# Performance work log

Measured on AMD Instinct MI355X. Metric: run time of the kernel, lower is better.

Reference implementation:

```python
import jax, jax.numpy as jnp
import numpy as np

USER_VOCAB = 1_000_000
MOVIE_VOCAB = 100_000
EMB_DIM = 64
BATCH = 65536
H1, H2 = 256, 128  # over_arch_layer_sizes


def setup_inputs() -> dict:
    key = jax.random.key(0)
    ks = jax.random.split(key, 10)
    inv = 1.0 / np.sqrt(EMB_DIM)
    return {
        "user_ids": jax.random.randint(ks[0], (BATCH,), 0, USER_VOCAB),
        "movie_ids": jax.random.randint(ks[1], (BATCH,), 0, MOVIE_VOCAB),
        "emb_user": jax.random.normal(ks[2], (USER_VOCAB, EMB_DIM), jnp.float32) * inv,
        "emb_movie": jax.random.normal(ks[3], (MOVIE_VOCAB, EMB_DIM), jnp.float32) * inv,
        "W1": jax.random.normal(ks[4], (EMB_DIM, H1), jnp.float32) * (1.0 / np.sqrt(EMB_DIM)),
        "b1": jnp.zeros((H1,), jnp.float32),
        "W2": jax.random.normal(ks[5], (H1, H2), jnp.float32) * (1.0 / np.sqrt(H1)),
        "b2": jnp.zeros((H2,), jnp.float32),
        "W3": jax.random.normal(ks[6], (H2, 1), jnp.float32) * (1.0 / np.sqrt(H2)),
        "b3": jnp.zeros((1,), jnp.float32),
    }


def reference(user_ids, movie_ids, emb_user, emb_movie, W1, b1, W2, b2, W3, b3):
    B = user_ids.shape[0]
    # sparse gather per feature (hotness = 1)
    eu = emb_user[user_ids]    # [B, D]
    em = emb_movie[movie_ids]  # [B, D]
    # concat jagged outputs along rows, matching torch.cat(..., dim=0)
    x = jnp.concatenate([eu, em], axis=0)  # [2B, D]
    h = jax.nn.relu(x @ W1 + b1)
    h = jax.nn.relu(h @ W2 + b2)
    p = h @ W3 + b3                        # [2B, 1]
    # view(num_features, batch).t().sum(-1) -> sum over features per sample
    return p.reshape(2, B).sum(axis=0)     # [B]
```

## Files before the change

kernel.cpp:

```cpp
#include <hip/hip_runtime.h>


typedef __attribute__((ext_vector_type(8))) short bf16x8;
typedef __attribute__((ext_vector_type(4))) float f32x4;

__device__ __forceinline__ unsigned int cvt_pk(float lo, float hi) {
  unsigned int r;
  asm("v_cvt_pk_bf16_f32 %0, %1, %2" : "=v"(r) : "v"(lo), "v"(hi));
  return r;
}

__global__ __launch_bounds__(512, 2) void movielens_mlp(
    const int* __restrict__ uids, const int* __restrict__ mids,
    const float* __restrict__ EU, const float* __restrict__ EM,
    const float* __restrict__ W1, const float* __restrict__ B1,
    const float* __restrict__ W2, const float* __restrict__ B2,
    const float* __restrict__ W3, const float* __restrict__ B3,
    float* __restrict__ out) {
  __shared__ __align__(16) unsigned short w1f[16 * 2 * 512];
  __shared__ __align__(16) unsigned short w2f[8 * 8 * 512];

  const int tid = threadIdx.x;
  const int lane = tid & 63, wv = tid >> 6;
  const int m = lane & 15, g = lane >> 4;

  const int sbase = blockIdx.x * 256 + wv * 32;
  const int su = sbase + m, sv = su + 16;

  const float* rp[4];
  rp[0] = EU + (size_t)uids[su] * 64;
  rp[1] = EU + (size_t)uids[sv] * 64;
  rp[2] = EM + (size_t)mids[su] * 64;
  rp[3] = EM + (size_t)mids[sv] * 64;
  float4 xr[4][2][2];
#pragma unroll
  for (int mt = 0; mt < 4; ++mt)
#pragma unroll
    for (int kt = 0; kt < 2; ++kt) {
      xr[mt][kt][0] = *(const float4*)(rp[mt] + kt * 32 + 8 * g);
      xr[mt][kt][1] = *(const float4*)(rp[mt] + kt * 32 + 8 * g + 4);
    }

  {
    const int u = tid & 63;
#pragma unroll
    for (int pass = 0; pass < 2; ++pass) {
      const int qd = (tid >> 6) + 8 * pass;
      const float* src = W1 + (qd * 4) * 256 + 4 * u;
      const float4 r0 = *(const float4*)(src);
      const float4 r1 = *(const float4*)(src + 256);
      const float4 r2 = *(const float4*)(src + 512);
      const float4 r3 = *(const float4*)(src + 768);
      const float c0[4] = {r0.x, r0.y, r0.z, r0.w};
      const float c1[4] = {r1.x, r1.y, r1.z, r1.w};
      const float c2[4] = {r2.x, r2.y, r2.z, r2.w};
      const float c3[4] = {r3.x, r3.y, r3.z, r3.w};
      const int kt = qd >> 3, gg = (qd >> 1) & 3, bo = (qd & 1) * 4;
#pragma unroll
      for (int p = 0; p < 4; ++p) {
        const int n = 4 * u + p;
        const int hq = n >> 5, cl = n & 31;
        const int nt = (cl >> 2) & 1, mm = 4 * (cl >> 3) + (cl & 3);
        const int fi = hq * 4 + nt * 2 + kt;
        uint2 pk;
        pk.x = cvt_pk(c0[p], c1[p]);
        pk.y = cvt_pk(c2[p], c3[p]);
        *(uint2*)&w1f[fi * 512 + (gg * 16 + mm) * 8 + bo] = pk;
      }
    }
    const int u2 = tid & 31;
#pragma unroll
    for (int pass = 0; pass < 4; ++pass) {
      const int qd = (tid >> 5) + 16 * pass;
      const float* src = W2 + (qd * 4) * 128 + 4 * u2;
      const float4 r0 = *(const float4*)(src);
      const float4 r1 = *(const float4*)(src + 128);
      const float4 r2 = *(const float4*)(src + 256);
      const float4 r3 = *(const float4*)(src + 384);
      const float c0[4] = {r0.x, r0.y, r0.z, r0.w};
      const float c1[4] = {r1.x, r1.y, r1.z, r1.w};
      const float c2[4] = {r2.x, r2.y, r2.z, r2.w};
      const float c3[4] = {r3.x, r3.y, r3.z, r3.w};
      const int hq2 = qd >> 3, gg = (qd >> 1) & 3, bo = (qd & 1) * 4;
#pragma unroll
      for (int p = 0; p < 4; ++p) {
        const int n = 4 * u2 + p, nt2 = n >> 4, mm = n & 15;
        uint2 pk;
        pk.x = cvt_pk(c0[p], c1[p]);
        pk.y = cvt_pk(c2[p], c3[p]);
        *(uint2*)&w2f[(nt2 * 8 + hq2) * 512 + (gg * 16 + mm) * 8 + bo] = pk;
      }
    }
  }

  bf16x8 xf[4][2];
#pragma unroll
  for (int mt = 0; mt < 4; ++mt)
#pragma unroll
    for (int kt = 0; kt < 2; ++kt) {
      const float4 a = xr[mt][kt][0], b = xr[mt][kt][1];
      uint4 t;
      t.x = cvt_pk(a.x, a.y);
      t.y = cvt_pk(a.z, a.w);
      t.z = cvt_pk(b.x, b.y);
      t.w = cvt_pk(b.z, b.w);
      xf[mt][kt] = __builtin_bit_cast(bf16x8, t);
    }
  __syncthreads();

  f32x4 acc2[4][8];
#pragma unroll
  for (int nt2 = 0; nt2 < 8; ++nt2) {
    const float4 bv = *(const float4*)(B2 + nt2 * 16 + 4 * g);
#pragma unroll
    for (int mt = 0; mt < 4; ++mt) {
      acc2[mt][nt2][0] = bv.x; acc2[mt][nt2][1] = bv.y;
      acc2[mt][nt2][2] = bv.z; acc2[mt][nt2][3] = bv.w;
    }
  }

#pragma unroll 2
  for (int hq = 0; hq < 8; ++hq) {
    uint4 hw[4];
#pragma unroll
    for (int nt = 0; nt < 2; ++nt) {
      const int fb = (hq * 4 + nt * 2) * 512;
      const bf16x8 wa0 = *(const bf16x8*)&w1f[fb + lane * 8];
      const bf16x8 wa1 = *(const bf16x8*)&w1f[fb + 512 + lane * 8];
      const float4 b1v = *(const float4*)(B1 + hq * 32 + 8 * g + 4 * nt);
#pragma unroll
      for (int mt = 0; mt < 4; ++mt) {
        f32x4 acc;
        acc[0] = b1v.x; acc[1] = b1v.y; acc[2] = b1v.z; acc[3] = b1v.w;
        acc = __builtin_amdgcn_mfma_f32_16x16x32_bf16(wa0, xf[mt][0], acc, 0, 0, 0);
        acc = __builtin_amdgcn_mfma_f32_16x16x32_bf16(wa1, xf[mt][1], acc, 0, 0, 0);
        const unsigned int wlo = cvt_pk(fmaxf(acc[0], 0.f), fmaxf(acc[1], 0.f));
        const unsigned int whi = cvt_pk(fmaxf(acc[2], 0.f), fmaxf(acc[3], 0.f));
        if (nt == 0) { hw[mt].x = wlo; hw[mt].y = whi; }
        else         { hw[mt].z = wlo; hw[mt].w = whi; }
      }
    }
#pragma unroll
    for (int nt2 = 0; nt2 < 8; ++nt2) {
      const bf16x8 w2v = *(const bf16x8*)&w2f[(nt2 * 8 + hq) * 512 + lane * 8];
#pragma unroll
      for (int mt = 0; mt < 4; ++mt)
        acc2[mt][nt2] = __builtin_amdgcn_mfma_f32_16x16x32_bf16(
            w2v, __builtin_bit_cast(bf16x8, hw[mt]), acc2[mt][nt2], 0, 0, 0);
    }
  }

  const float b3v = B3[0];
  float part[4] = {0.f, 0.f, 0.f, 0.f};
#pragma unroll
  for (int nt2 = 0; nt2 < 8; ++nt2) {
    const float4 w3v = *(const float4*)(W3 + nt2 * 16 + 4 * g);
#pragma unroll
    for (int mt = 0; mt < 4; ++mt) {
      const f32x4 c = acc2[mt][nt2];
      part[mt] += fmaxf(c[0], 0.f) * w3v.x + fmaxf(c[1], 0.f) * w3v.y +
                  fmaxf(c[2], 0.f) * w3v.z + fmaxf(c[3], 0.f) * w3v.w;
    }
  }
#pragma unroll
  for (int mt = 0; mt < 4; ++mt) {
    part[mt] += __shfl_xor(part[mt], 16, 64);
    part[mt] += __shfl_xor(part[mt], 32, 64);
  }
  if (lane < 16) {
    out[sbase + lane] = part[0] + part[2] + 2.f * b3v;
  } else if (lane < 32) {
    out[sbase + lane] = part[1] + part[3] + 2.f * b3v;
  }
}

extern "C" void kernel_launch(void* const* d_in, const int* in_sizes, int n_in,
                              void* d_out, int out_size, void* d_ws, size_t ws_size,
                              hipStream_t stream) {
  const int* uids = (const int*)d_in[0];
  const int* mids = (const int*)d_in[1];
  const float* EU = (const float*)d_in[2];
  const float* EM = (const float*)d_in[3];
  const float* W1 = (const float*)d_in[4];
  const float* B1 = (const float*)d_in[5];
  const float* W2 = (const float*)d_in[6];
  const float* B2 = (const float*)d_in[7];
  const float* W3 = (const float*)d_in[8];
  const float* B3 = (const float*)d_in[9];
  float* out = (float*)d_out;

  const int B = in_sizes[0];
  const int nblk = B / 256;
  hipLaunchKernelGGL(movielens_mlp, dim3(nblk), dim3(512), 0, stream,
                     uids, mids, EU, EM, W1, B1, W2, B2, W3, B3, out);
}
```

Baseline: 22.25 us.

## Pre-convert MLP weights once in a prep kernel and stream them via async LDS loads

```diff
diff --git a/kernel.cpp b/kernel.cpp
--- a/kernel.cpp
+++ b/kernel.cpp
@@ -10,21 +10,73 @@
   return r;
 }
 
-__global__ __launch_bounds__(512, 2) void movielens_mlp(
+__global__ __launch_bounds__(512) void prep_weights(
+    const float* __restrict__ W1, const float* __restrict__ W2,
+    unsigned short* __restrict__ w1g, unsigned short* __restrict__ w2g) {
+  const int tid = threadIdx.x;
+  const int b = blockIdx.x;
+  if (b < 2) {
+    const int u = tid & 63;
+    const int qd = (tid >> 6) + 8 * b;
+    const float* src = W1 + (qd * 4) * 256 + 4 * u;
+    const float4 r0 = *(const float4*)(src);
+    const float4 r1 = *(const float4*)(src + 256);
+    const float4 r2 = *(const float4*)(src + 512);
+    const float4 r3 = *(const float4*)(src + 768);
+    const float c0[4] = {r0.x, r0.y, r0.z, r0.w};
+    const float c1[4] = {r1.x, r1.y, r1.z, r1.w};
+    const float c2[4] = {r2.x, r2.y, r2.z, r2.w};
+    const float c3[4] = {r3.x, r3.y, r3.z, r3.w};
+    const int kt = qd >> 3, gg = (qd >> 1) & 3, bo = (qd & 1) * 4;
+#pragma unroll
+    for (int p = 0; p < 4; ++p) {
+      const int n = 4 * u + p;
+      const int hq = n >> 5, cl = n & 31;
+      const int nt = (cl >> 2) & 1, mm = 4 * (cl >> 3) + (cl & 3);
+      const int fi = hq * 4 + nt * 2 + kt;
+      uint2 pk;
+      pk.x = cvt_pk(c0[p], c1[p]);
+      pk.y = cvt_pk(c2[p], c3[p]);
+      *(uint2*)&w1g[fi * 512 + (gg * 16 + mm) * 8 + bo] = pk;
+    }
+  } else {
+    const int u2 = tid & 31;
+    const int qd = (tid >> 5) + 16 * (b - 2);
+    const float* src = W2 + (qd * 4) * 128 + 4 * u2;
+    const float4 r0 = *(const float4*)(src);
+    const float4 r1 = *(const float4*)(src + 128);
+    const float4 r2 = *(const float4*)(src + 256);
+    const float4 r3 = *(const float4*)(src + 384);
+    const float c0[4] = {r0.x, r0.y, r0.z, r0.w};
+    const float c1[4] = {r1.x, r1.y, r1.z, r1.w};
+    const float c2[4] = {r2.x, r2.y, r2.z, r2.w};
+    const float c3[4] = {r3.x, r3.y, r3.z, r3.w};
+    const int hq2 = qd >> 3, gg = (qd >> 1) & 3, bo = (qd & 1) * 4;
+#pragma unroll
+    for (int p = 0; p < 4; ++p) {
+      const int n = 4 * u2 + p, nt2 = n >> 4, mm = n & 15;
+      uint2 pk;
+      pk.x = cvt_pk(c0[p], c1[p]);
+      pk.y = cvt_pk(c2[p], c3[p]);
+      *(uint2*)&w2g[(nt2 * 8 + hq2) * 512 + (gg * 16 + mm) * 8 + bo] = pk;
+    }
+  }
+}
+
+__global__ __launch_bounds__(256, 2) void movielens_mlp(
     const int* __restrict__ uids, const int* __restrict__ mids,
     const float* __restrict__ EU, const float* __restrict__ EM,
-    const float* __restrict__ W1, const float* __restrict__ B1,
-    const float* __restrict__ W2, const float* __restrict__ B2,
+    const unsigned short* __restrict__ w1g, const float* __restrict__ B1,
+    const unsigned short* __restrict__ w2g, const float* __restrict__ B2,
     const float* __restrict__ W3, const float* __restrict__ B3,
     float* __restrict__ out) {
-  __shared__ __align__(16) unsigned short w1f[16 * 2 * 512];
-  __shared__ __align__(16) unsigned short w2f[8 * 8 * 512];
+  __shared__ __align__(16) unsigned short w2f[64 * 512];
 
   const int tid = threadIdx.x;
   const int lane = tid & 63, wv = tid >> 6;
   const int m = lane & 15, g = lane >> 4;
 
-  const int sbase = blockIdx.x * 256 + wv * 32;
+  const int sbase = blockIdx.x * 128 + wv * 32;
   const int su = sbase + m, sv = su + 16;
 
   const float* rp[4];
@@ -41,56 +93,14 @@
       xr[mt][kt][1] = *(const float4*)(rp[mt] + kt * 32 + 8 * g + 4);
     }
 
-  {
-    const int u = tid & 63;
-#pragma unroll
-    for (int pass = 0; pass < 2; ++pass) {
-      const int qd = (tid >> 6) + 8 * pass;
-      const float* src = W1 + (qd * 4) * 256 + 4 * u;
-      const float4 r0 = *(const float4*)(src);
-      const float4 r1 = *(const float4*)(src + 256);
-      const float4 r2 = *(const float4*)(src + 512);
-      const float4 r3 = *(const float4*)(src + 768);
-      const float c0[4] = {r0.x, r0.y, r0.z, r0.w};
-      const float c1[4] = {r1.x, r1.y, r1.z, r1.w};
-      const float c2[4] = {r2.x, r2.y, r2.z, r2.w};
-      const float c3[4] = {r3.x, r3.y, r3.z, r3.w};
-      const int kt = qd >> 3, gg = (qd >> 1) & 3, bo = (qd & 1) * 4;
-#pragma unroll
-      for (int p = 0; p < 4; ++p) {
-        const int n = 4 * u + p;
-        const int hq = n >> 5, cl = n & 31;
-        const int nt = (cl >> 2) & 1, mm = 4 * (cl >> 3) + (cl & 3);
-        const int fi = hq * 4 + nt * 2 + kt;
-        uint2 pk;
-        pk.x = cvt_pk(c0[p], c1[p]);
-        pk.y = cvt_pk(c2[p], c3[p]);
-        *(uint2*)&w1f[fi * 512 + (gg * 16 + mm) * 8 + bo] = pk;
-      }
-    }
-    const int u2 = tid & 31;
-#pragma unroll
-    for (int pass = 0; pass < 4; ++pass) {
-      const int qd = (tid >> 5) + 16 * pass;
-      const float* src = W2 + (qd * 4) * 128 + 4 * u2;
-      const float4 r0 = *(const float4*)(src);
-      const float4 r1 = *(const float4*)(src + 128);
-      const float4 r2 = *(const float4*)(src + 256);
-      const float4 r3 = *(const float4*)(src + 384);
-      const float c0[4] = {r0.x, r0.y, r0.z, r0.w};
-      const float c1[4] = {r1.x, r1.y, r1.z, r1.w};
-      const float c2[4] = {r2.x, r2.y, r2.z, r2.w};
-      const float c3[4] = {r3.x, r3.y, r3.z, r3.w};
-      const int hq2 = qd >> 3, gg = (qd >> 1) & 3, bo = (qd & 1) * 4;
-#pragma unroll
-      for (int p = 0; p < 4; ++p) {
-        const int n = 4 * u2 + p, nt2 = n >> 4, mm = n & 15;
-        uint2 pk;
-        pk.x = cvt_pk(c0[p], c1[p]);
-        pk.y = cvt_pk(c2[p], c3[p]);
-        *(uint2*)&w2f[(nt2 * 8 + hq2) * 512 + (gg * 16 + mm) * 8 + bo] = pk;
-      }
-    }
+#pragma unroll
+  for (int f = 0; f < 16; ++f) {
+    const int fi = wv * 16 + f;
+    __builtin_amdgcn_global_load_lds(
+        (const __attribute__((address_space(1))) unsigned int*)(const void*)(
+            w2g + fi * 512 + lane * 8),
+        (__attribute__((address_space(3))) unsigned int*)(void*)(&w2f[fi * 512]),
+        16, 0, 0);
   }
 
   bf16x8 xf[4][2];
@@ -124,9 +134,9 @@
     uint4 hw[4];
 #pragma unroll
     for (int nt = 0; nt < 2; ++nt) {
-      const int fb = (hq * 4 + nt * 2) * 512;
-      const bf16x8 wa0 = *(const bf16x8*)&w1f[fb + lane * 8];
-      const bf16x8 wa1 = *(const bf16x8*)&w1f[fb + 512 + lane * 8];
+      const unsigned short* wp = w1g + (hq * 4 + nt * 2) * 512 + lane * 8;
+      const bf16x8 wa0 = *(const bf16x8*)(wp);
+      const bf16x8 wa1 = *(const bf16x8*)(wp + 512);
       const float4 b1v = *(const float4*)(B1 + hq * 32 + 8 * g + 4 * nt);
 #pragma unroll
       for (int mt = 0; mt < 4; ++mt) {
@@ -189,8 +199,14 @@
   const float* B3 = (const float*)d_in[9];
   float* out = (float*)d_out;
 
+  unsigned short* w1g = (unsigned short*)d_ws;
+  unsigned short* w2g = w1g + 16 * 1024;
+
+  hipLaunchKernelGGL(prep_weights, dim3(6), dim3(512), 0, stream,
+                     W1, W2, w1g, w2g);
+
   const int B = in_sizes[0];
-  const int nblk = B / 256;
-  hipLaunchKernelGGL(movielens_mlp, dim3(nblk), dim3(512), 0, stream,
-                     uids, mids, EU, EM, W1, B1, W2, B2, W3, B3, out);
-}
+  const int nblk = B / 128;
+  hipLaunchKernelGGL(movielens_mlp, dim3(nblk), dim3(256), 0, stream,
+                     uids, mids, EU, EM, w1g, B1, w2g, B2, W3, B3, out);
+}
```

New measurement: 25.79 us. 15.9% more time.

## Switch fused MLP to 32x32x16 bf16 MFMA tiles with repacked LDS layouts

Applied to the files above, without the earlier changes.

```diff
diff --git a/kernel.cpp b/kernel.cpp
--- a/kernel.cpp
+++ b/kernel.cpp
@@ -2,7 +2,7 @@
 
 
 typedef __attribute__((ext_vector_type(8))) short bf16x8;
-typedef __attribute__((ext_vector_type(4))) float f32x4;
+typedef __attribute__((ext_vector_type(16))) float f32x16;
 
 __device__ __forceinline__ unsigned int cvt_pk(float lo, float hi) {
   unsigned int r;
@@ -17,36 +17,35 @@
     const float* __restrict__ W2, const float* __restrict__ B2,
     const float* __restrict__ W3, const float* __restrict__ B3,
     float* __restrict__ out) {
-  __shared__ __align__(16) unsigned short w1f[16 * 2 * 512];
-  __shared__ __align__(16) unsigned short w2f[8 * 8 * 512];
+  __shared__ __align__(16) unsigned short w1f[32 * 512];
+  __shared__ __align__(16) unsigned short w2f[64 * 512];
 
   const int tid = threadIdx.x;
   const int lane = tid & 63, wv = tid >> 6;
-  const int m = lane & 15, g = lane >> 4;
+  const int m32 = lane & 31, H = lane >> 5;
 
   const int sbase = blockIdx.x * 256 + wv * 32;
-  const int su = sbase + m, sv = su + 16;
-
-  const float* rp[4];
-  rp[0] = EU + (size_t)uids[su] * 64;
-  rp[1] = EU + (size_t)uids[sv] * 64;
-  rp[2] = EM + (size_t)mids[su] * 64;
-  rp[3] = EM + (size_t)mids[sv] * 64;
-  float4 xr[4][2][2];
-#pragma unroll
-  for (int mt = 0; mt < 4; ++mt)
-#pragma unroll
-    for (int kt = 0; kt < 2; ++kt) {
-      xr[mt][kt][0] = *(const float4*)(rp[mt] + kt * 32 + 8 * g);
-      xr[mt][kt][1] = *(const float4*)(rp[mt] + kt * 32 + 8 * g + 4);
-    }
-
-  {
-    const int u = tid & 63;
-#pragma unroll
-    for (int pass = 0; pass < 2; ++pass) {
-      const int qd = (tid >> 6) + 8 * pass;
-      const float* src = W1 + (qd * 4) * 256 + 4 * u;
+  const int sid = sbase + m32;
+
+  const float* rowU = EU + (size_t)uids[sid] * 64;
+  const float* rowM = EM + (size_t)mids[sid] * 64;
+  float4 xr[2][4][2];
+#pragma unroll
+  for (int kk = 0; kk < 4; ++kk) {
+    xr[0][kk][0] = *(const float4*)(rowU + 16 * kk + 8 * H);
+    xr[0][kk][1] = *(const float4*)(rowU + 16 * kk + 8 * H + 4);
+    xr[1][kk][0] = *(const float4*)(rowM + 16 * kk + 8 * H);
+    xr[1][kk][1] = *(const float4*)(rowM + 16 * kk + 8 * H + 4);
+  }
+
+#pragma unroll
+  for (int i = 0; i < 6; ++i) {
+    const int u = tid + 512 * i;
+    const int cq = u & 7, bb = (u >> 3) & 1, hh = (u >> 4) & 1;
+    if (i < 2) {
+      const int fi = u >> 5;
+      const int ct = fi >> 2, kk = fi & 3;
+      const float* src = W1 + (16 * kk + 8 * hh + 4 * bb) * 256 + 32 * ct + 4 * cq;
       const float4 r0 = *(const float4*)(src);
       const float4 r1 = *(const float4*)(src + 256);
       const float4 r2 = *(const float4*)(src + 512);
@@ -55,24 +54,19 @@
       const float c1[4] = {r1.x, r1.y, r1.z, r1.w};
       const float c2[4] = {r2.x, r2.y, r2.z, r2.w};
       const float c3[4] = {r3.x, r3.y, r3.z, r3.w};
-      const int kt = qd >> 3, gg = (qd >> 1) & 3, bo = (qd & 1) * 4;
-#pragma unroll
-      for (int p = 0; p < 4; ++p) {
-        const int n = 4 * u + p;
-        const int hq = n >> 5, cl = n & 31;
-        const int nt = (cl >> 2) & 1, mm = 4 * (cl >> 3) + (cl & 3);
-        const int fi = hq * 4 + nt * 2 + kt;
+      const int slot0 = 32 * hh + 16 * (cq >> 2) + 8 * (cq & 1) + 4 * ((cq >> 1) & 1);
+#pragma unroll
+      for (int s = 0; s < 4; ++s) {
         uint2 pk;
-        pk.x = cvt_pk(c0[p], c1[p]);
-        pk.y = cvt_pk(c2[p], c3[p]);
-        *(uint2*)&w1f[fi * 512 + (gg * 16 + mm) * 8 + bo] = pk;
-      }
-    }
-    const int u2 = tid & 31;
-#pragma unroll
-    for (int pass = 0; pass < 4; ++pass) {
-      const int qd = (tid >> 5) + 16 * pass;
-      const float* src = W2 + (qd * 4) * 128 + 4 * u2;
+        pk.x = cvt_pk(c0[s], c1[s]);
+        pk.y = cvt_pk(c2[s], c3[s]);
+        *(uint2*)&w1f[fi * 512 + (slot0 + s) * 8 + 4 * bb] = pk;
+      }
+    } else {
+      const int v = u - 1024;
+      const int f2 = v >> 5;
+      const int ks = f2 >> 2, n2 = f2 & 3;
+      const float* src = W2 + (16 * ks + 8 * hh + 4 * bb) * 128 + 32 * n2 + 4 * cq;
       const float4 r0 = *(const float4*)(src);
       const float4 r1 = *(const float4*)(src + 128);
       const float4 r2 = *(const float4*)(src + 256);
@@ -81,97 +75,147 @@
       const float c1[4] = {r1.x, r1.y, r1.z, r1.w};
       const float c2[4] = {r2.x, r2.y, r2.z, r2.w};
       const float c3[4] = {r3.x, r3.y, r3.z, r3.w};
-      const int hq2 = qd >> 3, gg = (qd >> 1) & 3, bo = (qd & 1) * 4;
-#pragma unroll
-      for (int p = 0; p < 4; ++p) {
-        const int n = 4 * u2 + p, nt2 = n >> 4, mm = n & 15;
+      const int slot0 = 32 * hh + 4 * cq;
+#pragma unroll
+      for (int s = 0; s < 4; ++s) {
         uint2 pk;
-        pk.x = cvt_pk(c0[p], c1[p]);
-        pk.y = cvt_pk(c2[p], c3[p]);
-        *(uint2*)&w2f[(nt2 * 8 + hq2) * 512 + (gg * 16 + mm) * 8 + bo] = pk;
-      }
-    }
-  }
-
-  bf16x8 xf[4][2];
-#pragma unroll
-  for (int mt = 0; mt < 4; ++mt)
-#pragma unroll
-    for (int kt = 0; kt < 2; ++kt) {
-      const float4 a = xr[mt][kt][0], b = xr[mt][kt][1];
-      uint4 t;
-      t.x = cvt_pk(a.x, a.y);
-      t.y = cvt_pk(a.z, a.w);
-      t.z = cvt_pk(b.x, b.y);
-      t.w = cvt_pk(b.z, b.w);
-      xf[mt][kt] = __builtin_bit_cast(bf16x8, t);
+        pk.x = cvt_pk(c0[s], c1[s]);
+        pk.y = cvt_pk(c2[s], c3[s]);
+        *(uint2*)&w2f[f2 * 512 + (slot0 + s) * 8 + 4 * bb] = pk;
+      }
+    }
+  }
+
+  bf16x8 xf[2][4];
+#pragma unroll
+  for (int t = 0; t < 2; ++t)
+#pragma unroll
+    for (int kk = 0; kk < 4; ++kk) {
+      const float4 a = xr[t][kk][0], b = xr[t][kk][1];
+      uint4 w;
+      w.x = cvt_pk(a.x, a.y);
+      w.y = cvt_pk(a.z, a.w);
+      w.z = cvt_pk(b.x, b.y);
+      w.w = cvt_pk(b.z, b.w);
+      xf[t][kk] = __builtin_bit_cast(bf16x8, w);
     }
   __syncthreads();
 
-  f32x4 acc2[4][8];
-#pragma unroll
-  for (int nt2 = 0; nt2 < 8; ++nt2) {
-    const float4 bv = *(const float4*)(B2 + nt2 * 16 + 4 * g);
-#pragma unroll
-    for (int mt = 0; mt < 4; ++mt) {
-      acc2[mt][nt2][0] = bv.x; acc2[mt][nt2][1] = bv.y;
-      acc2[mt][nt2][2] = bv.z; acc2[mt][nt2][3] = bv.w;
-    }
-  }
+  f32x16 acc2[2][4];
+#pragma unroll
+  for (int n2 = 0; n2 < 4; ++n2)
+#pragma unroll
+    for (int rq = 0; rq < 4; ++rq) {
+      const float4 bq = *(const float4*)(B2 + 32 * n2 + 8 * rq + 4 * H);
+      const float bv[4] = {bq.x, bq.y, bq.z, bq.w};
+#pragma unroll
+      for (int s = 0; s < 4; ++s) {
+        acc2[0][n2][4 * rq + s] = bv[s];
+        acc2[1][n2][4 * rq + s] = bv[s];
+      }
+    }
+
+  bf16x8 a1[4];
+#pragma unroll
+  for (int kk = 0; kk < 4; ++kk)
+    a1[kk] = *(const bf16x8*)&w1f[kk * 512 + lane * 8];
 
 #pragma unroll 2
-  for (int hq = 0; hq < 8; ++hq) {
-    uint4 hw[4];
-#pragma unroll
-    for (int nt = 0; nt < 2; ++nt) {
-      const int fb = (hq * 4 + nt * 2) * 512;
-      const bf16x8 wa0 = *(const bf16x8*)&w1f[fb + lane * 8];
-      const bf16x8 wa1 = *(const bf16x8*)&w1f[fb + 512 + lane * 8];
-      const float4 b1v = *(const float4*)(B1 + hq * 32 + 8 * g + 4 * nt);
-#pragma unroll
-      for (int mt = 0; mt < 4; ++mt) {
-        f32x4 acc;
-        acc[0] = b1v.x; acc[1] = b1v.y; acc[2] = b1v.z; acc[3] = b1v.w;
-        acc = __builtin_amdgcn_mfma_f32_16x16x32_bf16(wa0, xf[mt][0], acc, 0, 0, 0);
-        acc = __builtin_amdgcn_mfma_f32_16x16x32_bf16(wa1, xf[mt][1], acc, 0, 0, 0);
-        const unsigned int wlo = cvt_pk(fmaxf(acc[0], 0.f), fmaxf(acc[1], 0.f));
-        const unsigned int whi = cvt_pk(fmaxf(acc[2], 0.f), fmaxf(acc[3], 0.f));
-        if (nt == 0) { hw[mt].x = wlo; hw[mt].y = whi; }
-        else         { hw[mt].z = wlo; hw[mt].w = whi; }
-      }
-    }
-#pragma unroll
-    for (int nt2 = 0; nt2 < 8; ++nt2) {
-      const bf16x8 w2v = *(const bf16x8*)&w2f[(nt2 * 8 + hq) * 512 + lane * 8];
-#pragma unroll
-      for (int mt = 0; mt < 4; ++mt)
-        acc2[mt][nt2] = __builtin_amdgcn_mfma_f32_16x16x32_bf16(
-            w2v, __builtin_bit_cast(bf16x8, hw[mt]), acc2[mt][nt2], 0, 0, 0);
-    }
-  }
-
-  const float b3v = B3[0];
-  float part[4] = {0.f, 0.f, 0.f, 0.f};
-#pragma unroll
-  for (int nt2 = 0; nt2 < 8; ++nt2) {
-    const float4 w3v = *(const float4*)(W3 + nt2 * 16 + 4 * g);
-#pragma unroll
-    for (int mt = 0; mt < 4; ++mt) {
-      const f32x4 c = acc2[mt][nt2];
-      part[mt] += fmaxf(c[0], 0.f) * w3v.x + fmaxf(c[1], 0.f) * w3v.y +
-                  fmaxf(c[2], 0.f) * w3v.z + fmaxf(c[3], 0.f) * w3v.w;
-    }
-  }
-#pragma unroll
-  for (int mt = 0; mt < 4; ++mt) {
-    part[mt] += __shfl_xor(part[mt], 16, 64);
-    part[mt] += __shfl_xor(part[mt], 32, 64);
-  }
-  if (lane < 16) {
-    out[sbase + lane] = part[0] + part[2] + 2.f * b3v;
-  } else if (lane < 32) {
-    out[sbase + lane] = part[1] + part[3] + 2.f * b3v;
-  }
+  for (int ct = 0; ct < 8; ++ct) {
+    f32x16 acc1a;
+    {
+      const float4 q0 = *(const float4*)(B1 + 32 * ct + 8 * H);
+      const float4 q1 = *(const float4*)(B1 + 32 * ct + 8 * H + 4);
+      const float4 q2 = *(const float4*)(B1 + 32 * ct + 8 * H + 16);
+      const float4 q3 = *(const float4*)(B1 + 32 * ct + 8 * H + 20);
+      acc1a[0]=q0.x; acc1a[1]=q0.y; acc1a[2]=q0.z; acc1a[3]=q0.w;
+      acc1a[4]=q1.x; acc1a[5]=q1.y; acc1a[6]=q1.z; acc1a[7]=q1.w;
+      acc1a[8]=q2.x; acc1a[9]=q2.y; acc1a[10]=q2.z; acc1a[11]=q2.w;
+      acc1a[12]=q3.x; acc1a[13]=q3.y; acc1a[14]=q3.z; acc1a[15]=q3.w;
+    }
+#pragma unroll
+    for (int kk = 0; kk < 4; ++kk)
+      acc1a = __builtin_amdgcn_mfma_f32_32x32x16_bf16(a1[kk], xf[0][kk], acc1a, 0, 0, 0);
+
+    bf16x8 w2v[8];
+#pragma unroll
+    for (int q = 0; q < 8; ++q)
+      w2v[q] = *(const bf16x8*)&w2f[(8 * ct + q) * 512 + lane * 8];
+
+    uint4 lo0, hi0;
+    lo0.x = cvt_pk(fmaxf(acc1a[0], 0.f), fmaxf(acc1a[1], 0.f));
+    lo0.y = cvt_pk(fmaxf(acc1a[2], 0.f), fmaxf(acc1a[3], 0.f));
+    lo0.z = cvt_pk(fmaxf(acc1a[4], 0.f), fmaxf(acc1a[5], 0.f));
+    lo0.w = cvt_pk(fmaxf(acc1a[6], 0.f), fmaxf(acc1a[7], 0.f));
+    hi0.x = cvt_pk(fmaxf(acc1a[8], 0.f), fmaxf(acc1a[9], 0.f));
+    hi0.y = cvt_pk(fmaxf(acc1a[10], 0.f), fmaxf(acc1a[11], 0.f));
+    hi0.z = cvt_pk(fmaxf(acc1a[12], 0.f), fmaxf(acc1a[13], 0.f));
+    hi0.w = cvt_pk(fmaxf(acc1a[14], 0.f), fmaxf(acc1a[15], 0.f));
+
+    f32x16 acc1b;
+    {
+      const float4 q0 = *(const float4*)(B1 + 32 * ct + 8 * H);
+      const float4 q1 = *(const float4*)(B1 + 32 * ct + 8 * H + 4);
+      const float4 q2 = *(const float4*)(B1 + 32 * ct + 8 * H + 16);
+      const float4 q3 = *(const float4*)(B1 + 32 * ct + 8 * H + 20);
+      acc1b[0]=q0.x; acc1b[1]=q0.y; acc1b[2]=q0.z; acc1b[3]=q0.w;
+      acc1b[4]=q1.x; acc1b[5]=q1.y; acc1b[6]=q1.z; acc1b[7]=q1.w;
+      acc1b[8]=q2.x; acc1b[9]=q2.y; acc1b[10]=q2.z; acc1b[11]=q2.w;
+      acc1b[12]=q3.x; acc1b[13]=q3.y; acc1b[14]=q3.z; acc1b[15]=q3.w;
+    }
+#pragma unroll
+    for (int kk = 0; kk < 4; ++kk)
+      acc1b = __builtin_amdgcn_mfma_f32_32x32x16_bf16(a1[kk], xf[1][kk], acc1b, 0, 0, 0);
+
+    if (ct < 7) {
+#pragma unroll
+      for (int kk = 0; kk < 4; ++kk)
+        a1[kk] = *(const bf16x8*)&w1f[((ct + 1) * 4 + kk) * 512 + lane * 8];
+    }
+
+#pragma unroll
+    for (int n2 = 0; n2 < 4; ++n2) {
+      acc2[0][n2] = __builtin_amdgcn_mfma_f32_32x32x16_bf16(
+          w2v[n2], __builtin_bit_cast(bf16x8, lo0), acc2[0][n2], 0, 0, 0);
+      acc2[0][n2] = __builtin_amdgcn_mfma_f32_32x32x16_bf16(
+          w2v[4 + n2], __builtin_bit_cast(bf16x8, hi0), acc2[0][n2], 0, 0, 0);
+    }
+
+    uint4 lo1, hi1;
+    lo1.x = cvt_pk(fmaxf(acc1b[0], 0.f), fmaxf(acc1b[1], 0.f));
+    lo1.y = cvt_pk(fmaxf(acc1b[2], 0.f), fmaxf(acc1b[3], 0.f));
+    lo1.z = cvt_pk(fmaxf(acc1b[4], 0.f), fmaxf(acc1b[5], 0.f));
+    lo1.w = cvt_pk(fmaxf(acc1b[6], 0.f), fmaxf(acc1b[7], 0.f));
+    hi1.x = cvt_pk(fmaxf(acc1b[8], 0.f), fmaxf(acc1b[9], 0.f));
+    hi1.y = cvt_pk(fmaxf(acc1b[10], 0.f), fmaxf(acc1b[11], 0.f));
+    hi1.z = cvt_pk(fmaxf(acc1b[12], 0.f), fmaxf(acc1b[13], 0.f));
+    hi1.w = cvt_pk(fmaxf(acc1b[14], 0.f), fmaxf(acc1b[15], 0.f));
+
+#pragma unroll
+    for (int n2 = 0; n2 < 4; ++n2) {
+      acc2[1][n2] = __builtin_amdgcn_mfma_f32_32x32x16_bf16(
+          w2v[n2], __builtin_bit_cast(bf16x8, lo1), acc2[1][n2], 0, 0, 0);
+      acc2[1][n2] = __builtin_amdgcn_mfma_f32_32x32x16_bf16(
+          w2v[4 + n2], __builtin_bit_cast(bf16x8, hi1), acc2[1][n2], 0, 0, 0);
+    }
+  }
+
+  float part = 0.f;
+#pragma unroll
+  for (int n2 = 0; n2 < 4; ++n2) {
+#pragma unroll
+    for (int rq = 0; rq < 4; ++rq) {
+      const float4 wq = *(const float4*)(W3 + 32 * n2 + 8 * rq + 4 * H);
+      const float wv4[4] = {wq.x, wq.y, wq.z, wq.w};
+#pragma unroll
+      for (int s = 0; s < 4; ++s) {
+        part += fmaxf(acc2[0][n2][4 * rq + s], 0.f) * wv4[s];
+        part += fmaxf(acc2[1][n2][4 * rq + s], 0.f) * wv4[s];
+      }
+    }
+  }
+  part += __shfl_xor(part, 32, 64);
+  if (lane < 32) out[sbase + lane] = part + 2.f * B3[0];
 }
 
 extern "C" void kernel_launch(void* const* d_in, const int* in_sizes, int n_in,
```

New measurement: 21.79 us. 2.1% less time.
